# Optimization experiments

Hardware: AMD Instinct MI355X
Metric: run time of the kernel (lower is better)

## Reference

```python
import jax, jax.numpy as jnp
import numpy as np

# LIF decay constants: alpha = exp(-dt/tau_syn), beta = exp(-dt/tau_mem)
ALPHA = float(np.exp(-0.001 / 0.01))   # ~0.9048
BETA = float(np.exp(-0.001 / 0.005))   # ~0.8187


@jax.custom_vjp
def spike_fn(x):
    # HeavisideSigmoidApprox: Heaviside forward, sigmoid-derivative surrogate backward
    return (x > 0).astype(x.dtype)

def _spike_fwd(x):
    return spike_fn(x), x

def _spike_bwd(x, g):
    s = jax.nn.sigmoid(x)
    return (g * s * (1.0 - s),)

spike_fn.defvjp(_spike_fwd, _spike_bwd)


def lif_layer(spikes_in, W, R):
    """spikes_in: [B,T,F] -> (spikes [B,T,H], potentials [B,T,H])"""
    h = jnp.einsum('btf,fo->bto', spikes_in, W)  # [B,T,H]
    B, T, H = h.shape
    zeros = jnp.zeros((B, H), h.dtype)

    def step(carry, h_t):
        cur, pot, spk = carry
        rec = spk @ R                      # recurrent current from previous spikes
        new_spk = spike_fn(pot - 1.0)      # threshold at 1.0
        active = 1.0 - jax.lax.stop_gradient(new_spk)  # reset: .detach() in torch
        new_cur = ALPHA * cur + h_t + rec
        new_pot = (BETA * pot + new_cur) * active
        return (new_cur, new_pot, new_spk), (new_pot, new_spk)

    _, (pots, spks) = jax.lax.scan(step, (zeros, zeros, zeros), jnp.swapaxes(h, 0, 1))
    return jnp.swapaxes(spks, 0, 1), jnp.swapaxes(pots, 0, 1)


def readout_rnn(spikes, Wout):
    """spikes: [B,T,H] -> output potentials [B,T+1,O] (leading zero record)"""
    h = jnp.einsum('btf,fo->bto', spikes, Wout)  # [B,T,O]
    B, T, O = h.shape
    zeros = jnp.zeros((B, O), h.dtype)

    def step(carry, h_t):
        cur, pot = carry
        cur = ALPHA * cur + h_t
        pot = BETA * pot + cur
        return (cur, pot), pot

    _, pots = jax.lax.scan(step, (zeros, zeros), jnp.swapaxes(h, 0, 1))
    return jnp.concatenate([zeros[:, None, :], jnp.swapaxes(pots, 0, 1)], axis=1)


def _xavier(key, shape):
    std = np.sqrt(2.0 / (shape[0] + shape[1]))
    return jax.random.normal(key, shape, dtype=jnp.float32) * std


def setup_inputs() -> dict:
    key = jax.random.key(0)
    ks = jax.random.split(key, 6)
    B, T, F, H, O = 256, 100, 256, 1024, 8
    return {
        'inputs': jax.random.normal(ks[0], (B, T, F), dtype=jnp.float32),
        'W0': _xavier(ks[1], (F, H)),
        'W1': _xavier(ks[2], (H, H)),
        'R0': _xavier(ks[3], (H, H)),
        'R1': _xavier(ks[4], (H, H)),
        'Wout': _xavier(ks[5], (H, O)),
    }


def reference(inputs, W0, W1, R0, R1, Wout):
    s1, v1 = lif_layer(inputs, W0, R0)
    s2, v2 = lif_layer(s1, W1, R1)
    out = readout_rnn(s2, Wout)  # [B, T+1, O]
    return (out, s1, s2, v1, v2)
```

## Files before the change

### kernel.cpp

```cpp
#include <hip/hip_runtime.h>


#define SNN_B 256
#define SNN_T 100
#define SNN_F 256
#define SNN_H 1024
#define SNN_O 8

#define ALPHA 0.9048374180359595f
#define BETA  0.8187307530779818f

__global__ __launch_bounds__(256) void gemm_f32(
    const float* __restrict__ A, const float* __restrict__ Bm,
    float* __restrict__ C, int M, int N, int K)
{
    __shared__ float As[16][68];
    __shared__ float Bs[16][64];

    const int tid = threadIdx.x;
    const int m0 = blockIdx.y * 64;
    const int n0 = blockIdx.x * 64;
    const int tm = tid >> 4;
    const int tn = tid & 15;

    const int lrowA = tid >> 2;
    const int lkA   = (tid & 3) * 4;
    const int lkB   = tid >> 4;
    const int lnB   = (tid & 15) * 4;

    float acc[4][4] = {};

    for (int k0 = 0; k0 < K; k0 += 16) {
        float4 a = *(const float4*)&A[(size_t)(m0 + lrowA) * K + k0 + lkA];
        As[lkA + 0][lrowA] = a.x;
        As[lkA + 1][lrowA] = a.y;
        As[lkA + 2][lrowA] = a.z;
        As[lkA + 3][lrowA] = a.w;
        *(float4*)&Bs[lkB][lnB] =
            *(const float4*)&Bm[(size_t)(k0 + lkB) * N + n0 + lnB];
        __syncthreads();
        #pragma unroll
        for (int k = 0; k < 16; ++k) {
            float4 av = *(const float4*)&As[k][tm * 4];
            float4 bv = *(const float4*)&Bs[k][tn * 4];
            float am[4] = {av.x, av.y, av.z, av.w};
            float bn[4] = {bv.x, bv.y, bv.z, bv.w};
            #pragma unroll
            for (int i = 0; i < 4; ++i)
                #pragma unroll
                for (int j = 0; j < 4; ++j)
                    acc[i][j] = fmaf(am[i], bn[j], acc[i][j]);
        }
        __syncthreads();
    }

    #pragma unroll
    for (int i = 0; i < 4; ++i) {
        float4 o = make_float4(acc[i][0], acc[i][1], acc[i][2], acc[i][3]);
        *(float4*)&C[(size_t)(m0 + tm * 4 + i) * N + n0 + tn * 4] = o;
    }
}


#define LIF_LOAD(Xa, Xb, Xc, Xd, Xe, Xf, Xg, Xh, cidx)                        \
    {                                                                         \
        const int4 ka_ = *(const int4*)&slist[(cidx) << 3];                   \
        const int4 kb_ = *(const int4*)&slist[((cidx) << 3) + 4];             \
        Xa = Rc[(size_t)ka_.x << 10];                                         \
        Xb = Rc[(size_t)ka_.y << 10];                                         \
        Xc = Rc[(size_t)ka_.z << 10];                                         \
        Xd = Rc[(size_t)ka_.w << 10];                                         \
        Xe = Rc[(size_t)kb_.x << 10];                                         \
        Xf = Rc[(size_t)kb_.y << 10];                                         \
        Xg = Rc[(size_t)kb_.z << 10];                                         \
        Xh = Rc[(size_t)kb_.w << 10];                                         \
    }

#define LIF_SUM(Xa, Xb, Xc, Xd, Xe, Xf, Xg, Xh)                               \
    {                                                                         \
        a0 += Xa; a0 += Xb; a0 += Xc; a0 += Xd;                               \
        a0 += Xe; a0 += Xf; a0 += Xg; a0 += Xh;                               \
    }

__global__ __launch_bounds__(1024) void lif_scan(
    const float* __restrict__ hbuf,
    const float* __restrict__ R,
    float* __restrict__ s_out,
    float* __restrict__ v_out)
{
    __shared__ __align__(16) int slist[SNN_H];
    __shared__ int wtot[16];
    __shared__ int sn;

    const int tid = threadIdx.x;
    const int b = blockIdx.x;
    const int wv = tid >> 6;
    const int lane = tid & 63;
    const float* __restrict__ Rc = R + tid;

    float cur = 0.f, pot = 0.f;

    if (tid == 0) sn = 0;
    __syncthreads();

    const float* hrow = hbuf + (size_t)b * SNN_T * SNN_H + tid;
    float*       srow = s_out + (size_t)b * SNN_T * SNN_H + tid;
    float*       vrow = v_out + (size_t)b * SNN_T * SNN_H + tid;

    for (int t = 0; t < SNN_T; ++t) {
        const float hv = *hrow;
        hrow += SNN_H;

        const int n = sn;
        float a0 = 0.f;
        int i = 0;
        const int nc = n >> 3;
        if (nc > 0) {
            float A0, A1, A2, A3, A4, A5, A6, A7;
            float B0, B1, B2, B3, B4, B5, B6, B7;
            LIF_LOAD(A0, A1, A2, A3, A4, A5, A6, A7, 0);
            int c = 1;
            for (; c + 1 < nc; c += 2) {
                LIF_LOAD(B0, B1, B2, B3, B4, B5, B6, B7, c);
                LIF_SUM(A0, A1, A2, A3, A4, A5, A6, A7);
                LIF_LOAD(A0, A1, A2, A3, A4, A5, A6, A7, c + 1);
                LIF_SUM(B0, B1, B2, B3, B4, B5, B6, B7);
            }
            if (c < nc) {
                LIF_LOAD(B0, B1, B2, B3, B4, B5, B6, B7, c);
                LIF_SUM(A0, A1, A2, A3, A4, A5, A6, A7);
                LIF_SUM(B0, B1, B2, B3, B4, B5, B6, B7);
            } else {
                LIF_SUM(A0, A1, A2, A3, A4, A5, A6, A7);
            }
            i = nc << 3;
        }
        for (; i < n; ++i)
            a0 += Rc[(size_t)slist[i] << 10];

        const bool p = (pot - 1.0f) > 0.0f;
        const float s = p ? 1.0f : 0.0f;
        cur = fmaf(ALPHA, cur, hv) + a0;
        pot = fmaf(BETA, pot, cur) * (1.0f - s);

        *srow = s;
        *vrow = pot;
        srow += SNN_H; vrow += SNN_H;

        const unsigned long long m = __ballot(p);
        const unsigned long long lt = (1ull << lane) - 1ull;
        const int lpre = __popcll(m & lt);
        if (lane == 0) wtot[wv] = __popcll(m);
        __syncthreads();
        int off = lpre;
        #pragma unroll
        for (int q = 0; q < 15; ++q)
            if (q < wv) off += wtot[q];
        if (p) slist[off] = tid;
        if (tid == 0) {
            int stot = 0;
            #pragma unroll
            for (int q = 0; q < 16; ++q) stot += wtot[q];
            sn = stot;
        }
        __syncthreads();
    }
}

__global__ __launch_bounds__(256) void readout_gemm(
    const float* __restrict__ s2in, const float* __restrict__ Wout,
    float* __restrict__ h3)
{
    const int gid = blockIdx.x * 256 + threadIdx.x;
    const int row = gid >> 3;
    const int o = gid & 7;
    const float* srow = s2in + (size_t)row * SNN_H;
    float acc = 0.f;
    for (int k = 0; k < SNN_H; k += 4) {
        float4 s = *(const float4*)&srow[k];
        acc = fmaf(s.x, Wout[(k + 0) * SNN_O + o], acc);
        acc = fmaf(s.y, Wout[(k + 1) * SNN_O + o], acc);
        acc = fmaf(s.z, Wout[(k + 2) * SNN_O + o], acc);
        acc = fmaf(s.w, Wout[(k + 3) * SNN_O + o], acc);
    }
    h3[(size_t)row * SNN_O + o] = acc;
}

__global__ __launch_bounds__(256) void readout_scan(
    const float* __restrict__ h3, float* __restrict__ out)
{
    const int gid = blockIdx.x * 256 + threadIdx.x;
    const int b = gid >> 3;
    const int o = gid & 7;
    float c = 0.f, p = 0.f;
    out[((size_t)b * (SNN_T + 1) + 0) * SNN_O + o] = 0.f;
    for (int t = 0; t < SNN_T; ++t) {
        c = fmaf(ALPHA, c, h3[((size_t)b * SNN_T + t) * SNN_O + o]);
        p = fmaf(BETA, p, c);
        out[((size_t)b * (SNN_T + 1) + t + 1) * SNN_O + o] = p;
    }
}

extern "C" void kernel_launch(void* const* d_in, const int* in_sizes, int n_in,
                              void* d_out, int out_size, void* d_ws, size_t ws_size,
                              hipStream_t stream)
{
    const float* X    = (const float*)d_in[0];
    const float* W0   = (const float*)d_in[1];
    const float* W1   = (const float*)d_in[2];
    const float* R0   = (const float*)d_in[3];
    const float* R1   = (const float*)d_in[4];
    const float* Wout = (const float*)d_in[5];

    const size_t BT_H = (size_t)SNN_B * SNN_T * SNN_H;
    float* out = (float*)d_out;
    float* s1  = out + (size_t)SNN_B * (SNN_T + 1) * SNN_O;
    float* s2  = s1 + BT_H;
    float* v1  = s2 + BT_H;
    float* v2  = v1 + BT_H;

    float* ws   = (float*)d_ws;
    float* hbuf = ws;
    float* h3   = hbuf + BT_H;

    const int M = SNN_B * SNN_T;

    gemm_f32<<<dim3(SNN_H / 64, M / 64), 256, 0, stream>>>(X, W0, hbuf, M, SNN_H, SNN_F);

    lif_scan<<<SNN_B, 1024, 0, stream>>>(hbuf, R0, s1, v1);

    gemm_f32<<<dim3(SNN_H / 64, M / 64), 256, 0, stream>>>(s1, W1, hbuf, M, SNN_H, SNN_H);

    lif_scan<<<SNN_B, 1024, 0, stream>>>(hbuf, R1, s2, v2);

    readout_gemm<<<(M * SNN_O) / 256, 256, 0, stream>>>(s2, Wout, h3);
    readout_scan<<<(SNN_B * SNN_O) / 256, 256, 0, stream>>>(h3, out);
}
```

Before: 3.172 ms.

## Enlarge GEMM tiles to 128x128 with 8x8 register blocking and double buffering

The fp32 GEMM moves from 64x64 tiles with 4x4 per-thread outputs to 128x128 tiles with 8x8 per-thread outputs. K-slices of 8 are double-buffered in shared memory, and the next global tile is prefetched into registers while the current one is computed. The goal is more reuse per shared-memory load and hidden global latency. The cost is higher register pressure and fewer blocks (200x8) to fill the GPU. The LIF scan also switches its recurrent-weight indexing to 32-bit unsigned shift/or instead of 64-bit pointer arithmetic, which should trim address math in the gather loop.

```diff
diff --git a/kernel.cpp b/kernel.cpp
--- a/kernel.cpp
+++ b/kernel.cpp
@@ -14,50 +14,72 @@
     const float* __restrict__ A, const float* __restrict__ Bm,
     float* __restrict__ C, int M, int N, int K)
 {
-    __shared__ float As[16][68];
-    __shared__ float Bs[16][64];
+    __shared__ float As[2][8][132];
+    __shared__ float Bs[2][8][132];
 
     const int tid = threadIdx.x;
-    const int m0 = blockIdx.y * 64;
-    const int n0 = blockIdx.x * 64;
-    const int tm = tid >> 4;
-    const int tn = tid & 15;
-
-    const int lrowA = tid >> 2;
-    const int lkA   = (tid & 3) * 4;
-    const int lkB   = tid >> 4;
-    const int lnB   = (tid & 15) * 4;
-
-    float acc[4][4] = {};
-
-    for (int k0 = 0; k0 < K; k0 += 16) {
-        float4 a = *(const float4*)&A[(size_t)(m0 + lrowA) * K + k0 + lkA];
-        As[lkA + 0][lrowA] = a.x;
-        As[lkA + 1][lrowA] = a.y;
-        As[lkA + 2][lrowA] = a.z;
-        As[lkA + 3][lrowA] = a.w;
-        *(float4*)&Bs[lkB][lnB] =
-            *(const float4*)&Bm[(size_t)(k0 + lkB) * N + n0 + lnB];
-        __syncthreads();
+    const int m0 = blockIdx.y * 128;
+    const int n0 = blockIdx.x * 128;
+    const int ty = tid >> 4;
+    const int tx = tid & 15;
+
+    const int arow = tid >> 1;
+    const int akq  = (tid & 1) * 4;
+    const int bkr  = tid >> 5;
+    const int bnq  = (tid & 31) * 4;
+
+    const float* Aptr = A + (size_t)(m0 + arow) * K + akq;
+    const float* Bptr = Bm + (size_t)bkr * N + n0 + bnq;
+
+    float4 ar = *(const float4*)Aptr;
+    float4 br = *(const float4*)Bptr;
+    As[0][akq + 0][arow] = ar.x;
+    As[0][akq + 1][arow] = ar.y;
+    As[0][akq + 2][arow] = ar.z;
+    As[0][akq + 3][arow] = ar.w;
+    *(float4*)&Bs[0][bkr][bnq] = br;
+    __syncthreads();
+
+    float acc[8][8] = {};
+    const int NK = K >> 3;
+
+    for (int kt = 0; kt < NK; ++kt) {
+        const int cur = kt & 1;
+        if (kt + 1 < NK) {
+            ar = *(const float4*)(Aptr + (kt + 1) * 8);
+            br = *(const float4*)(Bptr + (size_t)(kt + 1) * 8 * N);
+        }
         #pragma unroll
-        for (int k = 0; k < 16; ++k) {
-            float4 av = *(const float4*)&As[k][tm * 4];
-            float4 bv = *(const float4*)&Bs[k][tn * 4];
-            float am[4] = {av.x, av.y, av.z, av.w};
-            float bn[4] = {bv.x, bv.y, bv.z, bv.w};
+        for (int k = 0; k < 8; ++k) {
+            const float4 a0 = *(const float4*)&As[cur][k][ty * 8];
+            const float4 a1 = *(const float4*)&As[cur][k][ty * 8 + 4];
+            const float4 b0 = *(const float4*)&Bs[cur][k][tx * 8];
+            const float4 b1 = *(const float4*)&Bs[cur][k][tx * 8 + 4];
+            const float am[8] = {a0.x, a0.y, a0.z, a0.w, a1.x, a1.y, a1.z, a1.w};
+            const float bn[8] = {b0.x, b0.y, b0.z, b0.w, b1.x, b1.y, b1.z, b1.w};
             #pragma unroll
-            for (int i = 0; i < 4; ++i)
+            for (int i = 0; i < 8; ++i)
                 #pragma unroll
-                for (int j = 0; j < 4; ++j)
+                for (int j = 0; j < 8; ++j)
                     acc[i][j] = fmaf(am[i], bn[j], acc[i][j]);
         }
-        __syncthreads();
+        if (kt + 1 < NK) {
+            const int nxt = cur ^ 1;
+            __syncthreads();
+            As[nxt][akq + 0][arow] = ar.x;
+            As[nxt][akq + 1][arow] = ar.y;
+            As[nxt][akq + 2][arow] = ar.z;
+            As[nxt][akq + 3][arow] = ar.w;
+            *(float4*)&Bs[nxt][bkr][bnq] = br;
+            __syncthreads();
+        }
     }
 
     #pragma unroll
-    for (int i = 0; i < 4; ++i) {
-        float4 o = make_float4(acc[i][0], acc[i][1], acc[i][2], acc[i][3]);
-        *(float4*)&C[(size_t)(m0 + tm * 4 + i) * N + n0 + tn * 4] = o;
+    for (int i = 0; i < 8; ++i) {
+        float* crow = C + (size_t)(m0 + ty * 8 + i) * N + n0 + tx * 8;
+        *(float4*)crow = make_float4(acc[i][0], acc[i][1], acc[i][2], acc[i][3]);
+        *(float4*)(crow + 4) = make_float4(acc[i][4], acc[i][5], acc[i][6], acc[i][7]);
     }
 }
 
@@ -65,15 +87,15 @@
 #define LIF_LOAD(Xa, Xb, Xc, Xd, Xe, Xf, Xg, Xh, cidx)                        \
     {                                                                         \
         const int4 ka_ = *(const int4*)&slist[(cidx) << 3];                   \
-        const int4 kb_ = *(const int4*)&slist[((cidx) << 3) + 4];             \
-        Xa = Rc[(size_t)ka_.x << 10];                                         \
-        Xb = Rc[(size_t)ka_.y << 10];                                         \
-        Xc = Rc[(size_t)ka_.z << 10];                                         \
-        Xd = Rc[(size_t)ka_.w << 10];                                         \
-        Xe = Rc[(size_t)kb_.x << 10];                                         \
-        Xf = Rc[(size_t)kb_.y << 10];                                         \
-        Xg = Rc[(size_t)kb_.z << 10];                                         \
-        Xh = Rc[(size_t)kb_.w << 10];                                         \
+        const int4 kb_ = *(const int4*)&slist[(((cidx) << 3) + 4)];           \
+        Xa = R[((unsigned)ka_.x << 10) | ctid];                               \
+        Xb = R[((unsigned)ka_.y << 10) | ctid];                               \
+        Xc = R[((unsigned)ka_.z << 10) | ctid];                               \
+        Xd = R[((unsigned)ka_.w << 10) | ctid];                               \
+        Xe = R[((unsigned)kb_.x << 10) | ctid];                               \
+        Xf = R[((unsigned)kb_.y << 10) | ctid];                               \
+        Xg = R[((unsigned)kb_.z << 10) | ctid];                               \
+        Xh = R[((unsigned)kb_.w << 10) | ctid];                               \
     }
 
 #define LIF_SUM(Xa, Xb, Xc, Xd, Xe, Xf, Xg, Xh)                               \
@@ -93,10 +115,10 @@
     __shared__ int sn;
 
     const int tid = threadIdx.x;
+    const unsigned ctid = (unsigned)tid;
     const int b = blockIdx.x;
     const int wv = tid >> 6;
     const int lane = tid & 63;
-    const float* __restrict__ Rc = R + tid;
 
     float cur = 0.f, pot = 0.f;
 
@@ -136,7 +158,7 @@
             i = nc << 3;
         }
         for (; i < n; ++i)
-            a0 += Rc[(size_t)slist[i] << 10];
+            a0 += R[((unsigned)slist[i] << 10) | ctid];
 
         const bool p = (pot - 1.0f) > 0.0f;
         const float s = p ? 1.0f : 0.0f;
@@ -225,11 +247,11 @@
 
     const int M = SNN_B * SNN_T;
 
-    gemm_f32<<<dim3(SNN_H / 64, M / 64), 256, 0, stream>>>(X, W0, hbuf, M, SNN_H, SNN_F);
+    gemm_f32<<<dim3(SNN_H / 128, M / 128), 256, 0, stream>>>(X, W0, hbuf, M, SNN_H, SNN_F);
 
     lif_scan<<<SNN_B, 1024, 0, stream>>>(hbuf, R0, s1, v1);
 
-    gemm_f32<<<dim3(SNN_H / 64, M / 64), 256, 0, stream>>>(s1, W1, hbuf, M, SNN_H, SNN_H);
+    gemm_f32<<<dim3(SNN_H / 128, M / 128), 256, 0, stream>>>(s1, W1, hbuf, M, SNN_H, SNN_H);
 
     lif_scan<<<SNN_B, 1024, 0, stream>>>(hbuf, R1, s2, v2);
 
```

Measured after the change: 3.108 ms. 1.02x faster.
